# Optimization experiments

Hardware: AMD Instinct MI355X
Metric: run time of the kernel (lower is better)

The kernel has to match this reference:

```python
import jax, jax.numpy as jnp
import numpy as np

STRIDE = 1
PADDING = 0


def setup_inputs() -> dict:
    key = jax.random.key(0)
    k1, k2, k3 = jax.random.split(key, 3)
    B, E, Cin, Cout, H, W = 32, 8, 64, 64, 160, 160
    x = jax.random.normal(k1, (B, Cin, H, W), dtype=jnp.float32)
    alpha = jax.random.uniform(k2, (B, E), dtype=jnp.float32)
    kernel_embed = jax.random.normal(k3, (E, Cout, Cin, 1, 1), dtype=jnp.float32)
    return {"x": x, "alpha": alpha, "kernel_embed": kernel_embed}


def reference(x, alpha, kernel_embed):
    # Per-sample kernel mix: [B,E] x [E,O,I,kh,kw] -> [B,O,I,kh,kw]
    kernels = jnp.einsum('be,eoihw->boihw', alpha, kernel_embed)

    def conv_one(xi, ki):
        # xi: [Cin,H,W], ki: [Cout,Cin,kh,kw]
        out = jax.lax.conv_general_dilated(
            xi[None],  # [1,Cin,H,W]
            ki,
            window_strides=(STRIDE, STRIDE),
            padding=[(PADDING, PADDING), (PADDING, PADDING)],
            dimension_numbers=('NCHW', 'OIHW', 'NCHW'),
        )
        return out[0]  # [Cout,Ho,Wo]

    return jax.vmap(conv_one)(x, kernels)  # [B,Cout,Ho,Wo]
```

## Files before the change

### kernel.cpp

```cpp
#include <hip/hip_runtime.h>
#include <cstdint>
#include <cstddef>


#define PIX 25600
#define CIN 64
#define COUT 64
#define BATCH 32
#define NEXP 8
#define TILE_PX 128
#define TILES_PER_B (PIX / TILE_PX)

__device__ __forceinline__ void load_lds16(const float* g, float* l) {
  __builtin_amdgcn_global_load_lds(
      (__attribute__((address_space(1))) void*)(g),
      (__attribute__((address_space(3))) void*)(l), 16, 0, 0);
}

__global__ __launch_bounds__(256) void mix_kernel(
    const float* __restrict__ alpha, const float* __restrict__ ke,
    float* __restrict__ kt) {
  const int b = blockIdx.x >> 3;
  const int seg = blockIdx.x & 7;
  __shared__ float a[NEXP];
  if (threadIdx.x < NEXP) a[threadIdx.x] = alpha[b * NEXP + threadIdx.x];
  __syncthreads();
#pragma unroll
  for (int t = 0; t < 2; t++) {
    const int idx = seg * 512 + t * 256 + threadIdx.x;
    float s = 0.f;
#pragma unroll
    for (int e = 0; e < NEXP; e++) s += a[e] * ke[e * 4096 + idx];
    const int o = idx >> 6, i = idx & 63;
    kt[b * 4096 + i * 64 + o] = s;
  }
}

__global__ __launch_bounds__(256, 3) void conv_kernel(
    const float* __restrict__ x, const float* __restrict__ kt,
    float* __restrict__ out) {
  __shared__ float ks[CIN * COUT];
  __shared__ float xs[CIN * TILE_PX];

  const int bid = blockIdx.x;
  const int b = bid / TILES_PER_B;
  const int tile = bid - b * TILES_PER_B;
  const int P0 = tile * TILE_PX;

  const int tid = threadIdx.x;
  const int wave = tid >> 6;
  const int lane = tid & 63;
  const int tc = tid >> 5;
  const int tp = tid & 31;

  const float* xb = x + (size_t)b * CIN * PIX + P0;
  const float* kb = kt + b * 4096;

#pragma unroll
  for (int j = 0; j < 4; j++) {
    const int r = wave * 4 + j;
    load_lds16(kb + r * 256 + lane * 4, &ks[r * 256]);
  }

#pragma unroll
  for (int j = 0; j < 8; j++) {
    const int r = wave * 16 + j * 2;
    load_lds16(xb + (size_t)(r + (lane >> 5)) * PIX + (lane & 31) * 4,
               &xs[r * TILE_PX]);
  }

  float acc[8][4];
#pragma unroll
  for (int c = 0; c < 8; c++)
#pragma unroll
    for (int p = 0; p < 4; p++) acc[c][p] = 0.f;

  __syncthreads();

  const float* xp4 = xs + tp * 4;
  const float* kp = ks + tc * 8;
#pragma unroll 8
  for (int ii = 0; ii < CIN; ii++) {
    const float4 xv = *(const float4*)(xp4 + ii * TILE_PX);
    const float4 k0 = *(const float4*)(kp + ii * 64);
    const float4 k1 = *(const float4*)(kp + ii * 64 + 4);
    const float kc[8] = {k0.x, k0.y, k0.z, k0.w, k1.x, k1.y, k1.z, k1.w};
    const float xv4[4] = {xv.x, xv.y, xv.z, xv.w};
#pragma unroll
    for (int c = 0; c < 8; c++)
#pragma unroll
      for (int p = 0; p < 4; p++) acc[c][p] = fmaf(kc[c], xv4[p], acc[c][p]);
  }

  float* ob = out + ((size_t)(b * COUT + tc * 8)) * PIX + P0 + tp * 4;
#pragma unroll
  for (int c = 0; c < 8; c++) {
    *(float4*)(ob + (size_t)c * PIX) =
        make_float4(acc[c][0], acc[c][1], acc[c][2], acc[c][3]);
  }
}

extern "C" void kernel_launch(void* const* d_in, const int* in_sizes, int n_in,
                              void* d_out, int out_size, void* d_ws,
                              size_t ws_size, hipStream_t stream) {
  const float* x = (const float*)d_in[0];
  const float* alpha = (const float*)d_in[1];
  const float* ke = (const float*)d_in[2];
  float* out = (float*)d_out;
  float* kt = (float*)d_ws;

  mix_kernel<<<BATCH * 8, 256, 0, stream>>>(alpha, ke, kt);
  conv_kernel<<<BATCH * TILES_PER_B, 256, 0, stream>>>(x, kt, out);
}
```

Measured before the change: 351.1 us.

## Process multiple pixel tiles per block with double-buffered LDS prefetch

Each conv block now handles five consecutive pixel tiles instead of one. It loads the mixed kernel weights into LDS once and prefetches the next input tile into a second LDS buffer while computing the current one, using manual vmcnt waits and barriers. This amortizes the kernel-weight load and overlaps global loads with FMA work. It also doubles the input LDS footprint, lowers the occupancy target to two blocks per CU, and shrinks the grid, which may hurt latency hiding and load balance.

```diff
diff --git a/kernel.cpp b/kernel.cpp
--- a/kernel.cpp
+++ b/kernel.cpp
@@ -10,6 +10,8 @@
 #define NEXP 8
 #define TILE_PX 128
 #define TILES_PER_B (PIX / TILE_PX)
+#define TPB 5
+#define GROUPS (TILES_PER_B / TPB)
 
 __device__ __forceinline__ void load_lds16(const float* g, float* l) {
   __builtin_amdgcn_global_load_lds(
@@ -36,16 +38,16 @@
   }
 }
 
-__global__ __launch_bounds__(256, 3) void conv_kernel(
+__global__ __launch_bounds__(256, 2) void conv_kernel(
     const float* __restrict__ x, const float* __restrict__ kt,
     float* __restrict__ out) {
   __shared__ float ks[CIN * COUT];
-  __shared__ float xs[CIN * TILE_PX];
+  __shared__ float xs[2][CIN * TILE_PX];
 
   const int bid = blockIdx.x;
-  const int b = bid / TILES_PER_B;
-  const int tile = bid - b * TILES_PER_B;
-  const int P0 = tile * TILE_PX;
+  const int b = bid / GROUPS;
+  const int g = bid - b * GROUPS;
+  const int tile0 = g * TPB;
 
   const int tid = threadIdx.x;
   const int wave = tid >> 6;
@@ -53,7 +55,7 @@
   const int tc = tid >> 5;
   const int tp = tid & 31;
 
-  const float* xb = x + (size_t)b * CIN * PIX + P0;
+  const float* xb = x + (size_t)b * CIN * PIX;
   const float* kb = kt + b * 4096;
 
 #pragma unroll
@@ -62,41 +64,70 @@
     load_lds16(kb + r * 256 + lane * 4, &ks[r * 256]);
   }
 
+  {
+    const float* gs = xb + (size_t)tile0 * TILE_PX;
 #pragma unroll
-  for (int j = 0; j < 8; j++) {
-    const int r = wave * 16 + j * 2;
-    load_lds16(xb + (size_t)(r + (lane >> 5)) * PIX + (lane & 31) * 4,
-               &xs[r * TILE_PX]);
+    for (int j = 0; j < 8; j++) {
+      const int r = wave * 16 + j * 2;
+      load_lds16(gs + (size_t)(r + (lane >> 5)) * PIX + (lane & 31) * 4,
+                 &xs[0][r * TILE_PX]);
+    }
   }
 
-  float acc[8][4];
+  for (int t = 0; t < TPB; ++t) {
+    const int cur = t & 1;
+
+    if (t) {
+      __builtin_amdgcn_s_barrier();
+      asm volatile("" ::: "memory");
+    }
+
+    if (t + 1 < TPB) {
+      const float* gs = xb + (size_t)(tile0 + t + 1) * TILE_PX;
+      float* dst = xs[cur ^ 1];
 #pragma unroll
-  for (int c = 0; c < 8; c++)
-#pragma unroll
-    for (int p = 0; p < 4; p++) acc[c][p] = 0.f;
+      for (int j = 0; j < 8; j++) {
+        const int r = wave * 16 + j * 2;
+        load_lds16(gs + (size_t)(r + (lane >> 5)) * PIX + (lane & 31) * 4,
+                   dst + r * TILE_PX);
+      }
+    }
 
-  __syncthreads();
+    if (t == 0 || t + 1 == TPB) {
+      asm volatile("s_waitcnt vmcnt(8)" ::: "memory");
+    } else {
+      asm volatile("s_waitcnt vmcnt(16)" ::: "memory");
+    }
+    __builtin_amdgcn_s_barrier();
 
-  const float* xp4 = xs + tp * 4;
-  const float* kp = ks + tc * 8;
-#pragma unroll 8
-  for (int ii = 0; ii < CIN; ii++) {
-    const float4 xv = *(const float4*)(xp4 + ii * TILE_PX);
-    const float4 k0 = *(const float4*)(kp + ii * 64);
-    const float4 k1 = *(const float4*)(kp + ii * 64 + 4);
-    const float kc[8] = {k0.x, k0.y, k0.z, k0.w, k1.x, k1.y, k1.z, k1.w};
-    const float xv4[4] = {xv.x, xv.y, xv.z, xv.w};
+    float acc[8][4];
 #pragma unroll
     for (int c = 0; c < 8; c++)
 #pragma unroll
-      for (int p = 0; p < 4; p++) acc[c][p] = fmaf(kc[c], xv4[p], acc[c][p]);
-  }
+      for (int p = 0; p < 4; p++) acc[c][p] = 0.f;
 
-  float* ob = out + ((size_t)(b * COUT + tc * 8)) * PIX + P0 + tp * 4;
+    const float* xp4 = &xs[cur][tp * 4];
+    const float* kp = ks + tc * 8;
+#pragma unroll 8
+    for (int ii = 0; ii < CIN; ii++) {
+      const float4 xv = *(const float4*)(xp4 + ii * TILE_PX);
+      const float4 k0 = *(const float4*)(kp + ii * 64);
+      const float4 k1 = *(const float4*)(kp + ii * 64 + 4);
+      const float kc[8] = {k0.x, k0.y, k0.z, k0.w, k1.x, k1.y, k1.z, k1.w};
+      const float xv4[4] = {xv.x, xv.y, xv.z, xv.w};
 #pragma unroll
-  for (int c = 0; c < 8; c++) {
-    *(float4*)(ob + (size_t)c * PIX) =
-        make_float4(acc[c][0], acc[c][1], acc[c][2], acc[c][3]);
+      for (int c = 0; c < 8; c++)
+#pragma unroll
+        for (int p = 0; p < 4; p++) acc[c][p] = fmaf(kc[c], xv4[p], acc[c][p]);
+    }
+
+    float* ob = out + ((size_t)(b * COUT + tc * 8)) * PIX +
+                (size_t)(tile0 + t) * TILE_PX + tp * 4;
+#pragma unroll
+    for (int c = 0; c < 8; c++) {
+      *(float4*)(ob + (size_t)c * PIX) =
+          make_float4(acc[c][0], acc[c][1], acc[c][2], acc[c][3]);
+    }
   }
 }
 
@@ -110,5 +141,5 @@
   float* kt = (float*)d_ws;
 
   mix_kernel<<<BATCH * 8, 256, 0, stream>>>(alpha, ke, kt);
-  conv_kernel<<<BATCH * TILES_PER_B, 256, 0, stream>>>(x, kt, out);
+  conv_kernel<<<BATCH * GROUPS, 256, 0, stream>>>(x, kt, out);
 }
```

Result: slower. 378.2 us (+7.7%).
